# Kernel tuning notes

Measured on AMD Instinct MI355X. Metric: run time of the kernel, lower is better.

The kernel has to match this reference:

```python
import jax, jax.numpy as jnp
import numpy as np

N_NODES = 50000

def _sage(x, src, dst, Wl, bl, Wr):
    # PyG SAGEConv(aggr='mean'): out = lin_l(mean_{j in N(i)} x_j) + lin_r(x_i)
    msg = x[src]                                                    # [E, F] gather
    agg = jax.ops.segment_sum(msg, dst, num_segments=N_NODES)      # [N, F]
    cnt = jax.ops.segment_sum(jnp.ones((src.shape[0],), x.dtype), dst, num_segments=N_NODES)
    agg = agg / jnp.maximum(cnt, 1.0)[:, None]                     # mean aggregate
    return agg @ Wl + bl + x @ Wr                                   # lin_l has bias, lin_r does not


def setup_inputs() -> dict:
    key = jax.random.key(0)
    ks = jax.random.split(key, 14)
    d_in, d_h, d_out, n_edges = 128, 64, 4, 800000
    s = lambda k, shp, fan: jax.random.normal(k, shp, jnp.float32) * (1.0 / np.sqrt(fan))
    return {
        'x': jax.random.normal(ks[0], (N_NODES, d_in), jnp.float32),
        'edge_index': jax.random.randint(ks[1], (2, n_edges), 0, N_NODES, jnp.int64),
        'Wl1': s(ks[2], (d_in, d_h), d_in), 'bl1': jnp.zeros((d_h,), jnp.float32),
        'Wr1': s(ks[3], (d_in, d_h), d_in),
        'Wl2': s(ks[4], (d_h, d_h), d_h), 'bl2': jnp.zeros((d_h,), jnp.float32),
        'Wr2': s(ks[5], (d_h, d_h), d_h),
        'Wl3': s(ks[6], (d_h, d_h), d_h), 'bl3': jnp.zeros((d_h,), jnp.float32),
        'Wr3': s(ks[7], (d_h, d_h), d_h),
        'Wp': s(ks[8], (2 * d_h, d_out), 2 * d_h), 'bp': jnp.zeros((d_out,), jnp.float32),
    }


def reference(x, edge_index, Wl1, bl1, Wr1, Wl2, bl2, Wr2, Wl3, bl3, Wr3, Wp, bp):
    src, dst = edge_index[0], edge_index[1]
    # dropout is identity in eval mode
    h = jax.nn.elu(_sage(x, src, dst, Wl1, bl1, Wr1))
    h = jax.nn.elu(_sage(h, src, dst, Wl2, bl2, Wr2))
    h = jax.nn.elu(_sage(h, src, dst, Wl3, bl3, Wr3))
    edge_feat = jnp.concatenate([h[src], h[dst]], axis=1)  # [E, 2*hidden]
    return edge_feat @ Wp + bp                              # [E, output_dim]
```

## Files before the change

kernel.cpp:

```cpp
#include <hip/hip_runtime.h>
#include <hip/hip_bf16.h>

#define N_NODES 50000
#define N_EDGES 800000
#define D_IN 128
#define D_H 64
#define SCAN_BLOCKS 196
#define HIST_BLOCKS 3125
#define LIN1_BLOCKS 782
#define FRAG_BLOCKS 8
#define GL_BLOCKS 3125

#define F2L 0
#define F2R 4096
#define F3L 8192
#define F3R 12288
#define FRAG_TOTAL 16384

typedef short bf16x8 __attribute__((ext_vector_type(8)));
typedef float f32x4 __attribute__((ext_vector_type(4)));

__device__ __forceinline__ ushort f2bf(float f) {
    __hip_bfloat16 b = __float2bfloat16(f);
    return *reinterpret_cast<ushort*>(&b);
}
__device__ __forceinline__ float bf16_lo(unsigned int u) { return __uint_as_float(u << 16); }
__device__ __forceinline__ float bf16_hi(unsigned int u) { return __uint_as_float(u & 0xffff0000u); }

__device__ __forceinline__ void build_frag_one(const float* __restrict__ W, int local,
                                               ushort* __restrict__ frag, int fid) {
    int lane = local & 63;
    int ktnt = local >> 6;
    int kt = ktnt >> 2, nt = ktnt & 3;
    int quad = lane >> 4, col = lane & 15;
    ushort t0 = f2bf(W[(kt * 32 + quad * 8 + 0) * D_H + nt * 16 + col]);
    ushort t1 = f2bf(W[(kt * 32 + quad * 8 + 1) * D_H + nt * 16 + col]);
    ushort t2 = f2bf(W[(kt * 32 + quad * 8 + 2) * D_H + nt * 16 + col]);
    ushort t3 = f2bf(W[(kt * 32 + quad * 8 + 3) * D_H + nt * 16 + col]);
    ushort t4 = f2bf(W[(kt * 32 + quad * 8 + 4) * D_H + nt * 16 + col]);
    ushort t5 = f2bf(W[(kt * 32 + quad * 8 + 5) * D_H + nt * 16 + col]);
    ushort t6 = f2bf(W[(kt * 32 + quad * 8 + 6) * D_H + nt * 16 + col]);
    ushort t7 = f2bf(W[(kt * 32 + quad * 8 + 7) * D_H + nt * 16 + col]);
    uint4 v;
    v.x = (unsigned int)t0 | ((unsigned int)t1 << 16);
    v.y = (unsigned int)t2 | ((unsigned int)t3 << 16);
    v.z = (unsigned int)t4 | ((unsigned int)t5 << 16);
    v.w = (unsigned int)t6 | ((unsigned int)t7 << 16);
    *reinterpret_cast<uint4*>(frag + (size_t)fid * 8) = v;
}

__device__ __forceinline__ void lin1_body(int gwave, int lane, const float* __restrict__ hin,
                                          const ushort* fl, const ushort* fr,
                                          ushort* __restrict__ Y, ushort* __restrict__ Zb) {
    constexpr int KT = D_IN / 32;
    int m0 = gwave * 16;
    if (m0 >= N_NODES) return;
    int col = lane & 15;
    int quad = lane >> 4;

    f32x4 accl[4], accr[4];
#pragma unroll
    for (int nt = 0; nt < 4; ++nt) {
        accl[nt] = (f32x4){0.f, 0.f, 0.f, 0.f};
        accr[nt] = (f32x4){0.f, 0.f, 0.f, 0.f};
    }
    const float* arow = hin + (size_t)(m0 + col) * D_IN + quad * 8;
#pragma unroll
    for (int kt = 0; kt < KT; ++kt) {
        float4 a_lo = *reinterpret_cast<const float4*>(arow + kt * 32);
        float4 a_hi = *reinterpret_cast<const float4*>(arow + kt * 32 + 4);
        bf16x8 a;
        a[0] = (short)f2bf(a_lo.x); a[1] = (short)f2bf(a_lo.y);
        a[2] = (short)f2bf(a_lo.z); a[3] = (short)f2bf(a_lo.w);
        a[4] = (short)f2bf(a_hi.x); a[5] = (short)f2bf(a_hi.y);
        a[6] = (short)f2bf(a_hi.z); a[7] = (short)f2bf(a_hi.w);
#pragma unroll
        for (int nt = 0; nt < 4; ++nt) {
            size_t off = (size_t)((kt * 4 + nt) * 64 + lane) * 8;
            bf16x8 bl = __builtin_bit_cast(bf16x8, *reinterpret_cast<const uint4*>(fl + off));
            bf16x8 br = __builtin_bit_cast(bf16x8, *reinterpret_cast<const uint4*>(fr + off));
            accl[nt] = __builtin_amdgcn_mfma_f32_16x16x32_bf16(a, bl, accl[nt], 0, 0, 0);
            accr[nt] = __builtin_amdgcn_mfma_f32_16x16x32_bf16(a, br, accr[nt], 0, 0, 0);
        }
    }
#pragma unroll
    for (int reg = 0; reg < 4; ++reg) {
        size_t r = (size_t)(m0 + quad * 4 + reg) * D_H;
        ushort* yp = Y + r;
        ushort* zp = Zb + r;
#pragma unroll
        for (int nt = 0; nt < 4; ++nt) {
            yp[nt * 16 + col] = f2bf(accl[nt][reg]);
            zp[nt * 16 + col] = f2bf(accr[nt][reg]);
        }
    }
}

__global__ void k1_kernel(const float* __restrict__ x,
                          const float* __restrict__ Wl1, const float* __restrict__ Wr1,
                          const float* __restrict__ Wl2, const float* __restrict__ Wr2,
                          const float* __restrict__ Wl3, const float* __restrict__ Wr3,
                          const int* __restrict__ dstv, int* __restrict__ cnt,
                          ushort* __restrict__ rank, ushort* __restrict__ wfrag,
                          ushort* __restrict__ Y, ushort* __restrict__ Zb) {
    __shared__ ushort fl[8192];
    __shared__ ushort fr[8192];
    if (blockIdx.x < LIN1_BLOCKS) {
#pragma unroll
        for (int i = 0; i < 4; ++i) {
            int local = i * 256 + threadIdx.x;
            build_frag_one(Wl1, local, fl, local);
            build_frag_one(Wr1, local, fr, local);
        }
        __syncthreads();
        int gwave = (blockIdx.x * 256 + threadIdx.x) >> 6;
        lin1_body(gwave, threadIdx.x & 63, x, fl, fr, Y, Zb);
    } else if (blockIdx.x < LIN1_BLOCKS + FRAG_BLOCKS) {
        int fid = (blockIdx.x - LIN1_BLOCKS) * 256 + threadIdx.x;
        const float* W; int base;
        if (fid < 512)       { W = Wl2; base = 0; }
        else if (fid < 1024) { W = Wr2; base = 512; }
        else if (fid < 1536) { W = Wl3; base = 1024; }
        else                 { W = Wr3; base = 1536; }
        build_frag_one(W, fid - base, wfrag, fid);
    } else {
        int e = (blockIdx.x - LIN1_BLOCKS - FRAG_BLOCKS) * 256 + threadIdx.x;
        if (e < N_EDGES) {
            int r = atomicAdd(&cnt[dstv[e]], 1);
            rank[e] = (ushort)r;
        }
    }
}

__global__ void scan_partial(const int* __restrict__ cnt, int* __restrict__ blockSums) {
    __shared__ int s[256];
    int i = blockIdx.x * 256 + threadIdx.x;
    s[threadIdx.x] = (i < N_NODES) ? cnt[i] : 0;
    __syncthreads();
    for (int off = 128; off > 0; off >>= 1) {
        if (threadIdx.x < off) s[threadIdx.x] += s[threadIdx.x + off];
        __syncthreads();
    }
    if (threadIdx.x == 0) blockSums[blockIdx.x] = s[0];
}

__global__ void scan_final(const int* __restrict__ cnt, const int* __restrict__ blockSums,
                           int* __restrict__ row_ptr) {
    __shared__ int s[256];
    __shared__ int bs[256];
    int t = threadIdx.x;
    bs[t] = (t < SCAN_BLOCKS) ? blockSums[t] : 0;
    int i = blockIdx.x * 256 + t;
    s[t] = (i < N_NODES) ? cnt[i] : 0;
    __syncthreads();
    for (int off = 1; off < 256; off <<= 1) {
        int tmp1 = (t >= off) ? s[t - off] : 0;
        int tmp2 = (t >= off) ? bs[t - off] : 0;
        __syncthreads();
        s[t] += tmp1;
        bs[t] += tmp2;
        __syncthreads();
    }
    int blockExcl = (blockIdx.x > 0) ? bs[blockIdx.x - 1] : 0;
    int excl = blockExcl + ((t > 0) ? s[t - 1] : 0);
    if (i < N_NODES) row_ptr[i] = excl;
    if (i == 0) row_ptr[N_NODES] = N_EDGES;
}

__global__ void fill_kernel(const int* __restrict__ srcv, const int* __restrict__ dstv,
                            const ushort* __restrict__ rank, const int* __restrict__ row_ptr,
                            ushort* __restrict__ csr_src) {
    int e = blockIdx.x * 256 + threadIdx.x;
    if (e < N_EDGES) {
        int d = dstv[e];
        int pos = row_ptr[d] + (int)rank[e];
        csr_src[pos] = (ushort)srcv[e];
    }
}

template <bool FUSE_PROJ>
__global__ void gather_lin_kernel(const ushort* __restrict__ Y, const ushort* __restrict__ Zb,
                                  const float* __restrict__ bl,
                                  const int* __restrict__ row_ptr, const ushort* __restrict__ csr_src,
                                  const ushort* __restrict__ fragWl, const ushort* __restrict__ fragWr,
                                  ushort* __restrict__ Ynext, ushort* __restrict__ Zbnext,
                                  const float* __restrict__ Wp, const float* __restrict__ bp,
                                  float* __restrict__ ps, float* __restrict__ pd) {
    __shared__ ushort Hs[16][72];
    int w = threadIdx.x >> 6;
    int lane = threadIdx.x & 63;
    int wv = (blockIdx.x << 2) + w;
    int n0 = wv << 2;
    int g = lane >> 4;
    int l = lane & 15;

    int rp[5];
#pragma unroll
    for (int i = 0; i < 5; ++i) rp[i] = row_ptr[n0 + i];
    int deg[4];
#pragma unroll
    for (int n = 0; n < 4; ++n) deg[n] = rp[n + 1] - rp[n];
    int maxdeg = deg[0];
#pragma unroll
    for (int n = 1; n < 4; ++n) maxdeg = deg[n] > maxdeg ? deg[n] : maxdeg;

    float acc[4][4] = {{0.f}};
    const uint2* __restrict__ Y2 = reinterpret_cast<const uint2*>(Y);

    for (int base = 0; base < maxdeg; base += 64) {
        int idxv[4];
#pragma unroll
        for (int n = 0; n < 4; ++n) idxv[n] = (int)csr_src[rp[n] + base + lane];
        int wend[4];
#pragma unroll
        for (int n = 0; n < 4; ++n) { wend[n] = deg[n] - base; if (wend[n] > 64) wend[n] = 64; }
        int kmax = wend[0];
#pragma unroll
        for (int n = 1; n < 4; ++n) kmax = wend[n] > kmax ? wend[n] : kmax;
        for (int k = 0; k < kmax; k += 16) {
            uint2 rr[4][4];
#pragma unroll
            for (int n = 0; n < 4; ++n)
#pragma unroll
                for (int j = 0; j < 4; ++j) {
                    int s = __shfl(idxv[n], k + 4 * j + g);
                    rr[n][j] = Y2[s * 16 + l];
                }
#pragma unroll
            for (int n = 0; n < 4; ++n)
#pragma unroll
                for (int j = 0; j < 4; ++j) {
                    if (k + 4 * j + g < wend[n]) {
                        acc[n][0] += bf16_lo(rr[n][j].x); acc[n][1] += bf16_hi(rr[n][j].x);
                        acc[n][2] += bf16_lo(rr[n][j].y); acc[n][3] += bf16_hi(rr[n][j].y);
                    }
                }
        }
    }

#pragma unroll
    for (int n = 0; n < 4; ++n)
#pragma unroll
        for (int f = 0; f < 4; ++f) {
            acc[n][f] += __shfl_xor(acc[n][f], 16);
            acc[n][f] += __shfl_xor(acc[n][f], 32);
        }

    int node = n0 + g;
    float dgf = (g == 0) ? (float)deg[0] : (g == 1) ? (float)deg[1]
              : (g == 2) ? (float)deg[2] : (float)deg[3];
    float c0 = (g == 0) ? acc[0][0] : (g == 1) ? acc[1][0] : (g == 2) ? acc[2][0] : acc[3][0];
    float c1 = (g == 0) ? acc[0][1] : (g == 1) ? acc[1][1] : (g == 2) ? acc[2][1] : acc[3][1];
    float c2 = (g == 0) ? acc[0][2] : (g == 1) ? acc[1][2] : (g == 2) ? acc[2][2] : acc[3][2];
    float c3 = (g == 0) ? acc[0][3] : (g == 1) ? acc[1][3] : (g == 2) ? acc[2][3] : acc[3][3];
    float inv = 1.0f / fmaxf(dgf, 1.0f);
    float4 bv = reinterpret_cast<const float4*>(bl)[l];
    uint2 zr = reinterpret_cast<const uint2*>(Zb)[node * 16 + l];
    float v0 = c0 * inv + bv.x + bf16_lo(zr.x);
    float v1 = c1 * inv + bv.y + bf16_hi(zr.x);
    float v2 = c2 * inv + bv.z + bf16_lo(zr.y);
    float v3 = c3 * inv + bv.w + bf16_hi(zr.y);
    float o0 = v0 > 0.f ? v0 : expm1f(v0);
    float o1 = v1 > 0.f ? v1 : expm1f(v1);
    float o2 = v2 > 0.f ? v2 : expm1f(v2);
    float o3 = v3 > 0.f ? v3 : expm1f(v3);

    if constexpr (FUSE_PROJ) {
        float p0 = 0.f, p1 = 0.f, p2 = 0.f, p3 = 0.f;
        float q0 = 0.f, q1 = 0.f, q2 = 0.f, q3 = 0.f;
        float ov[4] = {o0, o1, o2, o3};
#pragma unroll
        for (int j = 0; j < 4; ++j) {
            int k = 4 * l + j;
            float4 wt = reinterpret_cast<const float4*>(Wp)[k];
            float4 wb = reinterpret_cast<const float4*>(Wp)[D_H + k];
            p0 += ov[j] * wt.x; p1 += ov[j] * wt.y; p2 += ov[j] * wt.z; p3 += ov[j] * wt.w;
            q0 += ov[j] * wb.x; q1 += ov[j] * wb.y; q2 += ov[j] * wb.z; q3 += ov[j] * wb.w;
        }
#pragma unroll
        for (int off = 1; off < 16; off <<= 1) {
            p0 += __shfl_xor(p0, off); p1 += __shfl_xor(p1, off);
            p2 += __shfl_xor(p2, off); p3 += __shfl_xor(p3, off);
            q0 += __shfl_xor(q0, off); q1 += __shfl_xor(q1, off);
            q2 += __shfl_xor(q2, off); q3 += __shfl_xor(q3, off);
        }
        if (l == 0) {
            float4 bpv = *reinterpret_cast<const float4*>(bp);
            float4 pv; pv.x = p0 + bpv.x; pv.y = p1 + bpv.y; pv.z = p2 + bpv.z; pv.w = p3 + bpv.w;
            float4 qv; qv.x = q0; qv.y = q1; qv.z = q2; qv.w = q3;
            reinterpret_cast<float4*>(ps)[node] = pv;
            reinterpret_cast<float4*>(pd)[node] = qv;
        }
    } else {
        ushort4 ob;
        ob.x = f2bf(o0); ob.y = f2bf(o1); ob.z = f2bf(o2); ob.w = f2bf(o3);
        int localrow = w * 4 + g;
        *reinterpret_cast<ushort4*>(&Hs[localrow][4 * l]) = ob;
        __syncthreads();

        int col = lane & 15;
        int quad = lane >> 4;
        bf16x8 blf0 = __builtin_bit_cast(bf16x8,
            *reinterpret_cast<const uint4*>(fragWl + (size_t)((0 * 4 + w) * 64 + lane) * 8));
        bf16x8 blf1 = __builtin_bit_cast(bf16x8,
            *reinterpret_cast<const uint4*>(fragWl + (size_t)((1 * 4 + w) * 64 + lane) * 8));
        bf16x8 brf0 = __builtin_bit_cast(bf16x8,
            *reinterpret_cast<const uint4*>(fragWr + (size_t)((0 * 4 + w) * 64 + lane) * 8));
        bf16x8 brf1 = __builtin_bit_cast(bf16x8,
            *reinterpret_cast<const uint4*>(fragWr + (size_t)((1 * 4 + w) * 64 + lane) * 8));
        bf16x8 a0 = __builtin_bit_cast(bf16x8,
            *reinterpret_cast<const uint4*>(&Hs[col][quad * 8]));
        bf16x8 a1 = __builtin_bit_cast(bf16x8,
            *reinterpret_cast<const uint4*>(&Hs[col][32 + quad * 8]));
        f32x4 accl = {0.f,0.f,0.f,0.f};
        f32x4 accr = {0.f,0.f,0.f,0.f};
        accl = __builtin_amdgcn_mfma_f32_16x16x32_bf16(a0, blf0, accl, 0, 0, 0);
        accl = __builtin_amdgcn_mfma_f32_16x16x32_bf16(a1, blf1, accl, 0, 0, 0);
        accr = __builtin_amdgcn_mfma_f32_16x16x32_bf16(a0, brf0, accr, 0, 0, 0);
        accr = __builtin_amdgcn_mfma_f32_16x16x32_bf16(a1, brf1, accr, 0, 0, 0);

        int n0base = blockIdx.x * 16;
#pragma unroll
        for (int reg = 0; reg < 4; ++reg) {
            size_t r = (size_t)(n0base + quad * 4 + reg) * D_H + w * 16 + col;
            Ynext[r]  = f2bf(accl[reg]);
            Zbnext[r] = f2bf(accr[reg]);
        }
    }
}

__global__ void edge_final_kernel(const int* __restrict__ srcv, const int* __restrict__ dstv,
                                  const float* __restrict__ ps, const float* __restrict__ pd,
                                  float* __restrict__ out) {
    int e = blockIdx.x * 256 + threadIdx.x;
    if (e >= N_EDGES) return;
    float4 a = reinterpret_cast<const float4*>(ps)[srcv[e]];
    float4 b = reinterpret_cast<const float4*>(pd)[dstv[e]];
    float4 o;
    o.x = a.x + b.x;
    o.y = a.y + b.y;
    o.z = a.z + b.z;
    o.w = a.w + b.w;
    reinterpret_cast<float4*>(out)[e] = o;
}

extern "C" void kernel_launch(void* const* d_in, const int* in_sizes, int n_in,
                              void* d_out, int out_size, void* d_ws, size_t ws_size,
                              hipStream_t stream) {
    const float* x   = (const float*)d_in[0];
    const int*   ei  = (const int*)d_in[1];
    const float* Wl1 = (const float*)d_in[2];
    const float* bl1 = (const float*)d_in[3];
    const float* Wr1 = (const float*)d_in[4];
    const float* Wl2 = (const float*)d_in[5];
    const float* bl2 = (const float*)d_in[6];
    const float* Wr2 = (const float*)d_in[7];
    const float* Wl3 = (const float*)d_in[8];
    const float* bl3 = (const float*)d_in[9];
    const float* Wr3 = (const float*)d_in[10];
    const float* Wp  = (const float*)d_in[11];
    const float* bp  = (const float*)d_in[12];
    float* out = (float*)d_out;

    const int* srcv = ei;
    const int* dstv = ei + N_EDGES;

    int*   cnt       = (int*)d_ws;
    int*   blockSums = cnt + 50000;
    int*   row_ptr   = blockSums + 256;
    ushort* rank     = (ushort*)(row_ptr + 50001);
    ushort* csr_src  = rank + 800000;
    ushort* wfrag = (ushort*)(((uintptr_t)(csr_src + 800000 + 4096) + 127) & ~(uintptr_t)127);
    ushort* Y1  = (ushort*)(((uintptr_t)(wfrag + FRAG_TOTAL) + 127) & ~(uintptr_t)127);
    ushort* Zb1 = Y1 + (size_t)N_NODES * D_H;
    ushort* Y2  = Zb1 + (size_t)N_NODES * D_H;
    ushort* Zb2 = Y2 + (size_t)N_NODES * D_H;
    float* ps = (float*)(((uintptr_t)(Zb2 + (size_t)N_NODES * D_H) + 15) & ~(uintptr_t)15);
    float* pd = ps + (size_t)N_NODES * 4;

    hipMemsetAsync(cnt, 0, N_NODES * sizeof(int), stream);
    k1_kernel<<<LIN1_BLOCKS + FRAG_BLOCKS + HIST_BLOCKS, 256, 0, stream>>>(
        x, Wl1, Wr1, Wl2, Wr2, Wl3, Wr3, dstv, cnt, rank, wfrag, Y1, Zb1);

    scan_partial<<<SCAN_BLOCKS, 256, 0, stream>>>(cnt, blockSums);
    scan_final<<<SCAN_BLOCKS, 256, 0, stream>>>(cnt, blockSums, row_ptr);

    fill_kernel<<<HIST_BLOCKS, 256, 0, stream>>>(srcv, dstv, rank, row_ptr, csr_src);

    gather_lin_kernel<false><<<GL_BLOCKS, 256, 0, stream>>>(Y1, Zb1, bl1, row_ptr, csr_src,
                                                            wfrag + F2L, wfrag + F2R, Y2, Zb2,
                                                            nullptr, nullptr, nullptr, nullptr);

    gather_lin_kernel<false><<<GL_BLOCKS, 256, 0, stream>>>(Y2, Zb2, bl2, row_ptr, csr_src,
                                                            wfrag + F3L, wfrag + F3R, Y1, Zb1,
                                                            nullptr, nullptr, nullptr, nullptr);

    gather_lin_kernel<true><<<GL_BLOCKS, 256, 0, stream>>>(Y1, Zb1, bl3, row_ptr, csr_src,
                                                           nullptr, nullptr, nullptr, nullptr,
                                                           Wp, bp, ps, pd);

    edge_final_kernel<<<(N_EDGES + 255) / 256, 256, 0, stream>>>(srcv, dstv, ps, pd, out);
}
```

Measured before the change: 228.5 us.

## Sort nodes by degree bucket for balanced gather waves; split lin1 fragment staging

Builds a degree histogram and a counting-sort permutation of nodes into 64 degree buckets, and makes the gather/linear kernels process nodes in that permuted order. Each wave then handles four nodes of similar degree, which cuts divergence where lanes idle until the max degree in the group finishes. Outputs are scattered back through the permutation, which costs extra indirection and makes row writes non-contiguous. The layer-1 kernel also stages weight fragments in two halves to halve its shared memory, adding one more barrier.

```diff
diff --git a/kernel.cpp b/kernel.cpp
--- a/kernel.cpp
+++ b/kernel.cpp
@@ -10,6 +10,7 @@
 #define LIN1_BLOCKS 782
 #define FRAG_BLOCKS 8
 #define GL_BLOCKS 3125
+#define NBUCKET 64
 
 #define F2L 0
 #define F2R 4096
@@ -27,20 +28,17 @@
 __device__ __forceinline__ float bf16_lo(unsigned int u) { return __uint_as_float(u << 16); }
 __device__ __forceinline__ float bf16_hi(unsigned int u) { return __uint_as_float(u & 0xffff0000u); }
 
-__device__ __forceinline__ void build_frag_one(const float* __restrict__ W, int local,
-                                               ushort* __restrict__ frag, int fid) {
-    int lane = local & 63;
-    int ktnt = local >> 6;
-    int kt = ktnt >> 2, nt = ktnt & 3;
+__device__ __forceinline__ void build_frag_kt(const float* __restrict__ W, int ktA, int nt,
+                                              int lane, ushort* __restrict__ frag, int fid) {
     int quad = lane >> 4, col = lane & 15;
-    ushort t0 = f2bf(W[(kt * 32 + quad * 8 + 0) * D_H + nt * 16 + col]);
-    ushort t1 = f2bf(W[(kt * 32 + quad * 8 + 1) * D_H + nt * 16 + col]);
-    ushort t2 = f2bf(W[(kt * 32 + quad * 8 + 2) * D_H + nt * 16 + col]);
-    ushort t3 = f2bf(W[(kt * 32 + quad * 8 + 3) * D_H + nt * 16 + col]);
-    ushort t4 = f2bf(W[(kt * 32 + quad * 8 + 4) * D_H + nt * 16 + col]);
-    ushort t5 = f2bf(W[(kt * 32 + quad * 8 + 5) * D_H + nt * 16 + col]);
-    ushort t6 = f2bf(W[(kt * 32 + quad * 8 + 6) * D_H + nt * 16 + col]);
-    ushort t7 = f2bf(W[(kt * 32 + quad * 8 + 7) * D_H + nt * 16 + col]);
+    ushort t0 = f2bf(W[(ktA * 32 + quad * 8 + 0) * D_H + nt * 16 + col]);
+    ushort t1 = f2bf(W[(ktA * 32 + quad * 8 + 1) * D_H + nt * 16 + col]);
+    ushort t2 = f2bf(W[(ktA * 32 + quad * 8 + 2) * D_H + nt * 16 + col]);
+    ushort t3 = f2bf(W[(ktA * 32 + quad * 8 + 3) * D_H + nt * 16 + col]);
+    ushort t4 = f2bf(W[(ktA * 32 + quad * 8 + 4) * D_H + nt * 16 + col]);
+    ushort t5 = f2bf(W[(ktA * 32 + quad * 8 + 5) * D_H + nt * 16 + col]);
+    ushort t6 = f2bf(W[(ktA * 32 + quad * 8 + 6) * D_H + nt * 16 + col]);
+    ushort t7 = f2bf(W[(ktA * 32 + quad * 8 + 7) * D_H + nt * 16 + col]);
     uint4 v;
     v.x = (unsigned int)t0 | ((unsigned int)t1 << 16);
     v.y = (unsigned int)t2 | ((unsigned int)t3 << 16);
@@ -49,51 +47,11 @@
     *reinterpret_cast<uint4*>(frag + (size_t)fid * 8) = v;
 }
 
-__device__ __forceinline__ void lin1_body(int gwave, int lane, const float* __restrict__ hin,
-                                          const ushort* fl, const ushort* fr,
-                                          ushort* __restrict__ Y, ushort* __restrict__ Zb) {
-    constexpr int KT = D_IN / 32;
-    int m0 = gwave * 16;
-    if (m0 >= N_NODES) return;
-    int col = lane & 15;
-    int quad = lane >> 4;
-
-    f32x4 accl[4], accr[4];
-#pragma unroll
-    for (int nt = 0; nt < 4; ++nt) {
-        accl[nt] = (f32x4){0.f, 0.f, 0.f, 0.f};
-        accr[nt] = (f32x4){0.f, 0.f, 0.f, 0.f};
-    }
-    const float* arow = hin + (size_t)(m0 + col) * D_IN + quad * 8;
-#pragma unroll
-    for (int kt = 0; kt < KT; ++kt) {
-        float4 a_lo = *reinterpret_cast<const float4*>(arow + kt * 32);
-        float4 a_hi = *reinterpret_cast<const float4*>(arow + kt * 32 + 4);
-        bf16x8 a;
-        a[0] = (short)f2bf(a_lo.x); a[1] = (short)f2bf(a_lo.y);
-        a[2] = (short)f2bf(a_lo.z); a[3] = (short)f2bf(a_lo.w);
-        a[4] = (short)f2bf(a_hi.x); a[5] = (short)f2bf(a_hi.y);
-        a[6] = (short)f2bf(a_hi.z); a[7] = (short)f2bf(a_hi.w);
-#pragma unroll
-        for (int nt = 0; nt < 4; ++nt) {
-            size_t off = (size_t)((kt * 4 + nt) * 64 + lane) * 8;
-            bf16x8 bl = __builtin_bit_cast(bf16x8, *reinterpret_cast<const uint4*>(fl + off));
-            bf16x8 br = __builtin_bit_cast(bf16x8, *reinterpret_cast<const uint4*>(fr + off));
-            accl[nt] = __builtin_amdgcn_mfma_f32_16x16x32_bf16(a, bl, accl[nt], 0, 0, 0);
-            accr[nt] = __builtin_amdgcn_mfma_f32_16x16x32_bf16(a, br, accr[nt], 0, 0, 0);
-        }
-    }
-#pragma unroll
-    for (int reg = 0; reg < 4; ++reg) {
-        size_t r = (size_t)(m0 + quad * 4 + reg) * D_H;
-        ushort* yp = Y + r;
-        ushort* zp = Zb + r;
-#pragma unroll
-        for (int nt = 0; nt < 4; ++nt) {
-            yp[nt * 16 + col] = f2bf(accl[nt][reg]);
-            zp[nt * 16 + col] = f2bf(accr[nt][reg]);
-        }
-    }
+__device__ __forceinline__ void build_frag_one(const float* __restrict__ W, int local,
+                                               ushort* __restrict__ frag, int fid) {
+    int lane = local & 63;
+    int ktnt = local >> 6;
+    build_frag_kt(W, ktnt >> 2, ktnt & 3, lane, frag, fid);
 }
 
 __global__ void k1_kernel(const float* __restrict__ x,
@@ -103,18 +61,69 @@
                           const int* __restrict__ dstv, int* __restrict__ cnt,
                           ushort* __restrict__ rank, ushort* __restrict__ wfrag,
                           ushort* __restrict__ Y, ushort* __restrict__ Zb) {
-    __shared__ ushort fl[8192];
-    __shared__ ushort fr[8192];
+    __shared__ ushort fl[4096];
+    __shared__ ushort fr[4096];
     if (blockIdx.x < LIN1_BLOCKS) {
-#pragma unroll
-        for (int i = 0; i < 4; ++i) {
-            int local = i * 256 + threadIdx.x;
-            build_frag_one(Wl1, local, fl, local);
-            build_frag_one(Wr1, local, fr, local);
-        }
-        __syncthreads();
-        int gwave = (blockIdx.x * 256 + threadIdx.x) >> 6;
-        lin1_body(gwave, threadIdx.x & 63, x, fl, fr, Y, Zb);
+        int tid = threadIdx.x;
+        int lane = tid & 63;
+        int gwave = (blockIdx.x * 256 + tid) >> 6;
+        int m0 = gwave * 16;
+        int col = lane & 15;
+        int quad = lane >> 4;
+        f32x4 accl[4], accr[4];
+#pragma unroll
+        for (int nt = 0; nt < 4; ++nt) {
+            accl[nt] = (f32x4){0.f, 0.f, 0.f, 0.f};
+            accr[nt] = (f32x4){0.f, 0.f, 0.f, 0.f};
+        }
+        const float* arow = x + (size_t)(m0 + col) * D_IN + quad * 8;
+#pragma unroll
+        for (int s = 0; s < 2; ++s) {
+#pragma unroll
+            for (int i = 0; i < 2; ++i) {
+                int local = i * 256 + tid;
+                int ktnt = local >> 6;
+                int kt_l = ktnt >> 2, nt = ktnt & 3;
+                build_frag_kt(Wl1, 2 * s + kt_l, nt, local & 63, fl, local);
+                build_frag_kt(Wr1, 2 * s + kt_l, nt, local & 63, fr, local);
+            }
+            __syncthreads();
+            if (m0 < N_NODES) {
+#pragma unroll
+                for (int kt_l = 0; kt_l < 2; ++kt_l) {
+                    int ktA = 2 * s + kt_l;
+                    float4 a_lo = *reinterpret_cast<const float4*>(arow + ktA * 32);
+                    float4 a_hi = *reinterpret_cast<const float4*>(arow + ktA * 32 + 4);
+                    bf16x8 a;
+                    a[0] = (short)f2bf(a_lo.x); a[1] = (short)f2bf(a_lo.y);
+                    a[2] = (short)f2bf(a_lo.z); a[3] = (short)f2bf(a_lo.w);
+                    a[4] = (short)f2bf(a_hi.x); a[5] = (short)f2bf(a_hi.y);
+                    a[6] = (short)f2bf(a_hi.z); a[7] = (short)f2bf(a_hi.w);
+#pragma unroll
+                    for (int nt = 0; nt < 4; ++nt) {
+                        size_t off = (size_t)((kt_l * 4 + nt) * 64 + lane) * 8;
+                        bf16x8 bl = __builtin_bit_cast(bf16x8, *reinterpret_cast<const uint4*>(fl + off));
+                        bf16x8 br = __builtin_bit_cast(bf16x8, *reinterpret_cast<const uint4*>(fr + off));
+                        accl[nt] = __builtin_amdgcn_mfma_f32_16x16x32_bf16(a, bl, accl[nt], 0, 0, 0);
+                        accr[nt] = __builtin_amdgcn_mfma_f32_16x16x32_bf16(a, br, accr[nt], 0, 0, 0);
+                    }
+                }
+            }
+            if (s == 0) __syncthreads();
+        }
+        if (m0 < N_NODES) {
+#pragma unroll
+            for (int reg = 0; reg < 4; ++reg) {
+                size_t r = (size_t)(m0 + quad * 4 + reg) * D_H;
+                ushort* yp = Y + r;
+                ushort* zp = Zb + r;
+#pragma unroll
+                for (int nt = 0; nt < 4; ++nt) {
+                    yp[nt * 16 + col] = f2bf(accl[nt][reg]);
+                    zp[nt * 16 + col] = f2bf(accr[nt][reg]);
+                }
+            }
+        }
     } else if (blockIdx.x < LIN1_BLOCKS + FRAG_BLOCKS) {
         int fid = (blockIdx.x - LIN1_BLOCKS) * 256 + threadIdx.x;
         const float* W; int base;
@@ -132,11 +141,21 @@
     }
 }
 
-__global__ void scan_partial(const int* __restrict__ cnt, int* __restrict__ blockSums) {
+__global__ void scan_partial(const int* __restrict__ cnt, int* __restrict__ blockSums,
+                             int* __restrict__ dhist) {
     __shared__ int s[256];
+    __shared__ int h[NBUCKET];
     int i = blockIdx.x * 256 + threadIdx.x;
-    s[threadIdx.x] = (i < N_NODES) ? cnt[i] : 0;
+    int v = (i < N_NODES) ? cnt[i] : 0;
+    s[threadIdx.x] = v;
+    if (threadIdx.x < NBUCKET) h[threadIdx.x] = 0;
     __syncthreads();
+    if (i < N_NODES) {
+        int b = v < (NBUCKET - 1) ? v : (NBUCKET - 1);
+        atomicAdd(&h[b], 1);
+    }
+    __syncthreads();
+    if (threadIdx.x < NBUCKET) atomicAdd(&dhist[threadIdx.x], h[threadIdx.x]);
     for (int off = 128; off > 0; off >>= 1) {
         if (threadIdx.x < off) s[threadIdx.x] += s[threadIdx.x + off];
         __syncthreads();
@@ -145,26 +164,43 @@
 }
 
 __global__ void scan_final(const int* __restrict__ cnt, const int* __restrict__ blockSums,
-                           int* __restrict__ row_ptr) {
+                           const int* __restrict__ dhist, int* __restrict__ dcur,
+                           int* __restrict__ row_ptr, int* __restrict__ perm) {
     __shared__ int s[256];
     __shared__ int bs[256];
+    __shared__ int db[NBUCKET];
     int t = threadIdx.x;
-    bs[t] = (t < SCAN_BLOCKS) ? blockSums[t] : 0;
-    int i = blockIdx.x * 256 + t;
-    s[t] = (i < N_NODES) ? cnt[i] : 0;
-    __syncthreads();
-    for (int off = 1; off < 256; off <<= 1) {
-        int tmp1 = (t >= off) ? s[t - off] : 0;
-        int tmp2 = (t >= off) ? bs[t - off] : 0;
+    if (blockIdx.x < SCAN_BLOCKS) {
+        bs[t] = (t < SCAN_BLOCKS) ? blockSums[t] : 0;
+        int i = blockIdx.x * 256 + t;
+        s[t] = (i < N_NODES) ? cnt[i] : 0;
         __syncthreads();
-        s[t] += tmp1;
-        bs[t] += tmp2;
+        for (int off = 1; off < 256; off <<= 1) {
+            int tmp1 = (t >= off) ? s[t - off] : 0;
+            int tmp2 = (t >= off) ? bs[t - off] : 0;
+            __syncthreads();
+            s[t] += tmp1;
+            bs[t] += tmp2;
+            __syncthreads();
+        }
+        int blockExcl = (blockIdx.x > 0) ? bs[blockIdx.x - 1] : 0;
+        int excl = blockExcl + ((t > 0) ? s[t - 1] : 0);
+        if (i < N_NODES) row_ptr[i] = excl;
+        if (i == 0) row_ptr[N_NODES] = N_EDGES;
+    } else {
+        if (t == 0) {
+            int run = 0;
+            for (int j = 0; j < NBUCKET; ++j) { db[j] = run; run += dhist[j]; }
+        }
         __syncthreads();
-    }
-    int blockExcl = (blockIdx.x > 0) ? bs[blockIdx.x - 1] : 0;
-    int excl = blockExcl + ((t > 0) ? s[t - 1] : 0);
-    if (i < N_NODES) row_ptr[i] = excl;
-    if (i == 0) row_ptr[N_NODES] = N_EDGES;
+        int i = (blockIdx.x - SCAN_BLOCKS) * 256 + t;
+        if (i < N_NODES) {
+            int v = cnt[i];
+            int b = v < (NBUCKET - 1) ? v : (NBUCKET - 1);
+            int pos = db[b] + atomicAdd(&dcur[b], 1);
+            perm[pos] = i;
+        }
+    }
 }
 
 __global__ void fill_kernel(const int* __restrict__ srcv, const int* __restrict__ dstv,
@@ -182,11 +218,13 @@
 __global__ void gather_lin_kernel(const ushort* __restrict__ Y, const ushort* __restrict__ Zb,
                                   const float* __restrict__ bl,
                                   const int* __restrict__ row_ptr, const ushort* __restrict__ csr_src,
+                                  const int* __restrict__ perm,
                                   const ushort* __restrict__ fragWl, const ushort* __restrict__ fragWr,
                                   ushort* __restrict__ Ynext, ushort* __restrict__ Zbnext,
                                   const float* __restrict__ Wp, const float* __restrict__ bp,
                                   float* __restrict__ ps, float* __restrict__ pd) {
     __shared__ ushort Hs[16][72];
+    __shared__ int nids[16];
     int w = threadIdx.x >> 6;
     int lane = threadIdx.x & 63;
     int wv = (blockIdx.x << 2) + w;
@@ -194,12 +232,15 @@
     int g = lane >> 4;
     int l = lane & 15;
 
-    int rp[5];
-#pragma unroll
-    for (int i = 0; i < 5; ++i) rp[i] = row_ptr[n0 + i];
-    int deg[4];
-#pragma unroll
-    for (int n = 0; n < 4; ++n) deg[n] = rp[n + 1] - rp[n];
+    int nid[4];
+#pragma unroll
+    for (int n = 0; n < 4; ++n) nid[n] = perm[n0 + n];
+    int rplo[4], deg[4];
+#pragma unroll
+    for (int n = 0; n < 4; ++n) {
+        rplo[n] = row_ptr[nid[n]];
+        deg[n] = row_ptr[nid[n] + 1] - rplo[n];
+    }
     int maxdeg = deg[0];
 #pragma unroll
     for (int n = 1; n < 4; ++n) maxdeg = deg[n] > maxdeg ? deg[n] : maxdeg;
@@ -210,7 +251,7 @@
     for (int base = 0; base < maxdeg; base += 64) {
         int idxv[4];
 #pragma unroll
-        for (int n = 0; n < 4; ++n) idxv[n] = (int)csr_src[rp[n] + base + lane];
+        for (int n = 0; n < 4; ++n) idxv[n] = (int)csr_src[rplo[n] + base + lane];
         int wend[4];
 #pragma unroll
         for (int n = 0; n < 4; ++n) { wend[n] = deg[n] - base; if (wend[n] > 64) wend[n] = 64; }
@@ -246,7 +287,7 @@
             acc[n][f] += __shfl_xor(acc[n][f], 32);
         }
 
-    int node = n0 + g;
+    int node = (g == 0) ? nid[0] : (g == 1) ? nid[1] : (g == 2) ? nid[2] : nid[3];
     float dgf = (g == 0) ? (float)deg[0] : (g == 1) ? (float)deg[1]
               : (g == 2) ? (float)deg[2] : (float)deg[3];
     float c0 = (g == 0) ? acc[0][0] : (g == 1) ? acc[1][0] : (g == 2) ? acc[2][0] : acc[3][0];
@@ -296,6 +337,7 @@
         ob.x = f2bf(o0); ob.y = f2bf(o1); ob.z = f2bf(o2); ob.w = f2bf(o3);
         int localrow = w * 4 + g;
         *reinterpret_cast<ushort4*>(&Hs[localrow][4 * l]) = ob;
+        if (l == 0) nids[localrow] = node;
         __syncthreads();
 
         int col = lane & 15;
@@ -319,10 +361,10 @@
         accr = __builtin_amdgcn_mfma_f32_16x16x32_bf16(a0, brf0, accr, 0, 0, 0);
         accr = __builtin_amdgcn_mfma_f32_16x16x32_bf16(a1, brf1, accr, 0, 0, 0);
 
-        int n0base = blockIdx.x * 16;
 #pragma unroll
         for (int reg = 0; reg < 4; ++reg) {
-            size_t r = (size_t)(n0base + quad * 4 + reg) * D_H + w * 16 + col;
+            int orow = nids[quad * 4 + reg];
+            size_t r = (size_t)orow * D_H + w * 16 + col;
             Ynext[r]  = f2bf(accl[reg]);
             Zbnext[r] = f2bf(accr[reg]);
         }
@@ -366,9 +408,12 @@
     const int* dstv = ei + N_EDGES;
 
     int*   cnt       = (int*)d_ws;
-    int*   blockSums = cnt + 50000;
+    int*   dhist     = cnt + 50000;
+    int*   dcur      = dhist + 64;
+    int*   blockSums = dcur + 64;
     int*   row_ptr   = blockSums + 256;
-    ushort* rank     = (ushort*)(row_ptr + 50001);
+    int*   perm      = row_ptr + 50001;
+    ushort* rank     = (ushort*)(perm + 50000);
     ushort* csr_src  = rank + 800000;
     ushort* wfrag = (ushort*)(((uintptr_t)(csr_src + 800000 + 4096) + 127) & ~(uintptr_t)127);
     ushort* Y1  = (ushort*)(((uintptr_t)(wfrag + FRAG_TOTAL) + 127) & ~(uintptr_t)127);
@@ -378,24 +423,24 @@
     float* ps = (float*)(((uintptr_t)(Zb2 + (size_t)N_NODES * D_H) + 15) & ~(uintptr_t)15);
     float* pd = ps + (size_t)N_NODES * 4;
 
-    hipMemsetAsync(cnt, 0, N_NODES * sizeof(int), stream);
+    hipMemsetAsync(cnt, 0, (50000 + 128) * sizeof(int), stream);
     k1_kernel<<<LIN1_BLOCKS + FRAG_BLOCKS + HIST_BLOCKS, 256, 0, stream>>>(
         x, Wl1, Wr1, Wl2, Wr2, Wl3, Wr3, dstv, cnt, rank, wfrag, Y1, Zb1);
 
-    scan_partial<<<SCAN_BLOCKS, 256, 0, stream>>>(cnt, blockSums);
-    scan_final<<<SCAN_BLOCKS, 256, 0, stream>>>(cnt, blockSums, row_ptr);
+    scan_partial<<<SCAN_BLOCKS, 256, 0, stream>>>(cnt, blockSums, dhist);
+    scan_final<<<2 * SCAN_BLOCKS, 256, 0, stream>>>(cnt, blockSums, dhist, dcur, row_ptr, perm);
 
     fill_kernel<<<HIST_BLOCKS, 256, 0, stream>>>(srcv, dstv, rank, row_ptr, csr_src);
 
-    gather_lin_kernel<false><<<GL_BLOCKS, 256, 0, stream>>>(Y1, Zb1, bl1, row_ptr, csr_src,
+    gather_lin_kernel<false><<<GL_BLOCKS, 256, 0, stream>>>(Y1, Zb1, bl1, row_ptr, csr_src, perm,
                                                             wfrag + F2L, wfrag + F2R, Y2, Zb2,
                                                             nullptr, nullptr, nullptr, nullptr);
 
-    gather_lin_kernel<false><<<GL_BLOCKS, 256, 0, stream>>>(Y2, Zb2, bl2, row_ptr, csr_src,
+    gather_lin_kernel<false><<<GL_BLOCKS, 256, 0, stream>>>(Y2, Zb2, bl2, row_ptr, csr_src, perm,
                                                             wfrag + F3L, wfrag + F3R, Y1, Zb1,
                                                             nullptr, nullptr, nullptr, nullptr);
 
-    gather_lin_kernel<true><<<GL_BLOCKS, 256, 0, stream>>>(Y1, Zb1, bl3, row_ptr, csr_src,
+    gather_lin_kernel<true><<<GL_BLOCKS, 256, 0, stream>>>(Y1, Zb1, bl3, row_ptr, csr_src, perm,
                                                            nullptr, nullptr, nullptr, nullptr,
                                                            Wp, bp, ps, pd);
 
```

Result: slower. 339.2 us (+48.4%).

## Stage layer-1 weight fragments in two K halves and predicate gather accumulation

Applied to the files above, without the earlier changes.

The first-layer GEMM blocks now build the bf16 weight fragments in two K-halves, using half the shared memory, and interleave fragment construction with the MFMA work. The goal is higher occupancy and earlier start of compute in the lin1 path, at the cost of an extra barrier. In the aggregation kernel, the branchy conditional adds become mask-multiplied FMAs to avoid divergence. The bias and Zb loads are also hoisted ahead of the cross-lane reductions so their latency overlaps the shuffles.

```diff
diff --git a/kernel.cpp b/kernel.cpp
--- a/kernel.cpp
+++ b/kernel.cpp
@@ -27,20 +27,17 @@
 __device__ __forceinline__ float bf16_lo(unsigned int u) { return __uint_as_float(u << 16); }
 __device__ __forceinline__ float bf16_hi(unsigned int u) { return __uint_as_float(u & 0xffff0000u); }
 
-__device__ __forceinline__ void build_frag_one(const float* __restrict__ W, int local,
-                                               ushort* __restrict__ frag, int fid) {
-    int lane = local & 63;
-    int ktnt = local >> 6;
-    int kt = ktnt >> 2, nt = ktnt & 3;
+__device__ __forceinline__ void build_frag_kt(const float* __restrict__ W, int ktA, int nt,
+                                              int lane, ushort* __restrict__ frag, int fid) {
     int quad = lane >> 4, col = lane & 15;
-    ushort t0 = f2bf(W[(kt * 32 + quad * 8 + 0) * D_H + nt * 16 + col]);
-    ushort t1 = f2bf(W[(kt * 32 + quad * 8 + 1) * D_H + nt * 16 + col]);
-    ushort t2 = f2bf(W[(kt * 32 + quad * 8 + 2) * D_H + nt * 16 + col]);
-    ushort t3 = f2bf(W[(kt * 32 + quad * 8 + 3) * D_H + nt * 16 + col]);
-    ushort t4 = f2bf(W[(kt * 32 + quad * 8 + 4) * D_H + nt * 16 + col]);
-    ushort t5 = f2bf(W[(kt * 32 + quad * 8 + 5) * D_H + nt * 16 + col]);
-    ushort t6 = f2bf(W[(kt * 32 + quad * 8 + 6) * D_H + nt * 16 + col]);
-    ushort t7 = f2bf(W[(kt * 32 + quad * 8 + 7) * D_H + nt * 16 + col]);
+    ushort t0 = f2bf(W[(ktA * 32 + quad * 8 + 0) * D_H + nt * 16 + col]);
+    ushort t1 = f2bf(W[(ktA * 32 + quad * 8 + 1) * D_H + nt * 16 + col]);
+    ushort t2 = f2bf(W[(ktA * 32 + quad * 8 + 2) * D_H + nt * 16 + col]);
+    ushort t3 = f2bf(W[(ktA * 32 + quad * 8 + 3) * D_H + nt * 16 + col]);
+    ushort t4 = f2bf(W[(ktA * 32 + quad * 8 + 4) * D_H + nt * 16 + col]);
+    ushort t5 = f2bf(W[(ktA * 32 + quad * 8 + 5) * D_H + nt * 16 + col]);
+    ushort t6 = f2bf(W[(ktA * 32 + quad * 8 + 6) * D_H + nt * 16 + col]);
+    ushort t7 = f2bf(W[(ktA * 32 + quad * 8 + 7) * D_H + nt * 16 + col]);
     uint4 v;
     v.x = (unsigned int)t0 | ((unsigned int)t1 << 16);
     v.y = (unsigned int)t2 | ((unsigned int)t3 << 16);
@@ -49,51 +46,11 @@
     *reinterpret_cast<uint4*>(frag + (size_t)fid * 8) = v;
 }
 
-__device__ __forceinline__ void lin1_body(int gwave, int lane, const float* __restrict__ hin,
-                                          const ushort* fl, const ushort* fr,
-                                          ushort* __restrict__ Y, ushort* __restrict__ Zb) {
-    constexpr int KT = D_IN / 32;
-    int m0 = gwave * 16;
-    if (m0 >= N_NODES) return;
-    int col = lane & 15;
-    int quad = lane >> 4;
-
-    f32x4 accl[4], accr[4];
-#pragma unroll
-    for (int nt = 0; nt < 4; ++nt) {
-        accl[nt] = (f32x4){0.f, 0.f, 0.f, 0.f};
-        accr[nt] = (f32x4){0.f, 0.f, 0.f, 0.f};
-    }
-    const float* arow = hin + (size_t)(m0 + col) * D_IN + quad * 8;
-#pragma unroll
-    for (int kt = 0; kt < KT; ++kt) {
-        float4 a_lo = *reinterpret_cast<const float4*>(arow + kt * 32);
-        float4 a_hi = *reinterpret_cast<const float4*>(arow + kt * 32 + 4);
-        bf16x8 a;
-        a[0] = (short)f2bf(a_lo.x); a[1] = (short)f2bf(a_lo.y);
-        a[2] = (short)f2bf(a_lo.z); a[3] = (short)f2bf(a_lo.w);
-        a[4] = (short)f2bf(a_hi.x); a[5] = (short)f2bf(a_hi.y);
-        a[6] = (short)f2bf(a_hi.z); a[7] = (short)f2bf(a_hi.w);
-#pragma unroll
-        for (int nt = 0; nt < 4; ++nt) {
-            size_t off = (size_t)((kt * 4 + nt) * 64 + lane) * 8;
-            bf16x8 bl = __builtin_bit_cast(bf16x8, *reinterpret_cast<const uint4*>(fl + off));
-            bf16x8 br = __builtin_bit_cast(bf16x8, *reinterpret_cast<const uint4*>(fr + off));
-            accl[nt] = __builtin_amdgcn_mfma_f32_16x16x32_bf16(a, bl, accl[nt], 0, 0, 0);
-            accr[nt] = __builtin_amdgcn_mfma_f32_16x16x32_bf16(a, br, accr[nt], 0, 0, 0);
-        }
-    }
-#pragma unroll
-    for (int reg = 0; reg < 4; ++reg) {
-        size_t r = (size_t)(m0 + quad * 4 + reg) * D_H;
-        ushort* yp = Y + r;
-        ushort* zp = Zb + r;
-#pragma unroll
-        for (int nt = 0; nt < 4; ++nt) {
-            yp[nt * 16 + col] = f2bf(accl[nt][reg]);
-            zp[nt * 16 + col] = f2bf(accr[nt][reg]);
-        }
-    }
+__device__ __forceinline__ void build_frag_one(const float* __restrict__ W, int local,
+                                               ushort* __restrict__ frag, int fid) {
+    int lane = local & 63;
+    int ktnt = local >> 6;
+    build_frag_kt(W, ktnt >> 2, ktnt & 3, lane, frag, fid);
 }
 
 __global__ void k1_kernel(const float* __restrict__ x,
@@ -103,18 +60,69 @@
                           const int* __restrict__ dstv, int* __restrict__ cnt,
                           ushort* __restrict__ rank, ushort* __restrict__ wfrag,
                           ushort* __restrict__ Y, ushort* __restrict__ Zb) {
-    __shared__ ushort fl[8192];
-    __shared__ ushort fr[8192];
+    __shared__ ushort fl[4096];
+    __shared__ ushort fr[4096];
     if (blockIdx.x < LIN1_BLOCKS) {
-#pragma unroll
-        for (int i = 0; i < 4; ++i) {
-            int local = i * 256 + threadIdx.x;
-            build_frag_one(Wl1, local, fl, local);
-            build_frag_one(Wr1, local, fr, local);
-        }
-        __syncthreads();
-        int gwave = (blockIdx.x * 256 + threadIdx.x) >> 6;
-        lin1_body(gwave, threadIdx.x & 63, x, fl, fr, Y, Zb);
+        int tid = threadIdx.x;
+        int lane = tid & 63;
+        int gwave = (blockIdx.x * 256 + tid) >> 6;
+        int m0 = gwave * 16;
+        int col = lane & 15;
+        int quad = lane >> 4;
+        f32x4 accl[4], accr[4];
+#pragma unroll
+        for (int nt = 0; nt < 4; ++nt) {
+            accl[nt] = (f32x4){0.f, 0.f, 0.f, 0.f};
+            accr[nt] = (f32x4){0.f, 0.f, 0.f, 0.f};
+        }
+        const float* arow = x + (size_t)(m0 + col) * D_IN + quad * 8;
+#pragma unroll
+        for (int s = 0; s < 2; ++s) {
+#pragma unroll
+            for (int i = 0; i < 2; ++i) {
+                int local = i * 256 + tid;
+                int ktnt = local >> 6;
+                int kt_l = ktnt >> 2, nt = ktnt & 3;
+                build_frag_kt(Wl1, 2 * s + kt_l, nt, local & 63, fl, local);
+                build_frag_kt(Wr1, 2 * s + kt_l, nt, local & 63, fr, local);
+            }
+            __syncthreads();
+            if (m0 < N_NODES) {
+#pragma unroll
+                for (int kt_l = 0; kt_l < 2; ++kt_l) {
+                    int ktA = 2 * s + kt_l;
+                    float4 a_lo = *reinterpret_cast<const float4*>(arow + ktA * 32);
+                    float4 a_hi = *reinterpret_cast<const float4*>(arow + ktA * 32 + 4);
+                    bf16x8 a;
+                    a[0] = (short)f2bf(a_lo.x); a[1] = (short)f2bf(a_lo.y);
+                    a[2] = (short)f2bf(a_lo.z); a[3] = (short)f2bf(a_lo.w);
+                    a[4] = (short)f2bf(a_hi.x); a[5] = (short)f2bf(a_hi.y);
+                    a[6] = (short)f2bf(a_hi.z); a[7] = (short)f2bf(a_hi.w);
+#pragma unroll
+                    for (int nt = 0; nt < 4; ++nt) {
+                        size_t off = (size_t)((kt_l * 4 + nt) * 64 + lane) * 8;
+                        bf16x8 bl = __builtin_bit_cast(bf16x8, *reinterpret_cast<const uint4*>(fl + off));
+                        bf16x8 br = __builtin_bit_cast(bf16x8, *reinterpret_cast<const uint4*>(fr + off));
+                        accl[nt] = __builtin_amdgcn_mfma_f32_16x16x32_bf16(a, bl, accl[nt], 0, 0, 0);
+                        accr[nt] = __builtin_amdgcn_mfma_f32_16x16x32_bf16(a, br, accr[nt], 0, 0, 0);
+                    }
+                }
+            }
+            if (s == 0) __syncthreads();
+        }
+        if (m0 < N_NODES) {
+#pragma unroll
+            for (int reg = 0; reg < 4; ++reg) {
+                size_t r = (size_t)(m0 + quad * 4 + reg) * D_H;
+                ushort* yp = Y + r;
+                ushort* zp = Zb + r;
+#pragma unroll
+                for (int nt = 0; nt < 4; ++nt) {
+                    yp[nt * 16 + col] = f2bf(accl[nt][reg]);
+                    zp[nt * 16 + col] = f2bf(accr[nt][reg]);
+                }
+            }
+        }
     } else if (blockIdx.x < LIN1_BLOCKS + FRAG_BLOCKS) {
         int fid = (blockIdx.x - LIN1_BLOCKS) * 256 + threadIdx.x;
         const float* W; int base;
@@ -230,13 +238,18 @@
             for (int n = 0; n < 4; ++n)
 #pragma unroll
                 for (int j = 0; j < 4; ++j) {
-                    if (k + 4 * j + g < wend[n]) {
-                        acc[n][0] += bf16_lo(rr[n][j].x); acc[n][1] += bf16_hi(rr[n][j].x);
-                        acc[n][2] += bf16_lo(rr[n][j].y); acc[n][3] += bf16_hi(rr[n][j].y);
-                    }
+                    float m = (k + 4 * j + g < wend[n]) ? 1.0f : 0.0f;
+                    acc[n][0] = fmaf(m, bf16_lo(rr[n][j].x), acc[n][0]);
+                    acc[n][1] = fmaf(m, bf16_hi(rr[n][j].x), acc[n][1]);
+                    acc[n][2] = fmaf(m, bf16_lo(rr[n][j].y), acc[n][2]);
+                    acc[n][3] = fmaf(m, bf16_hi(rr[n][j].y), acc[n][3]);
                 }
         }
     }
+
+    int node = n0 + g;
+    float4 bv = reinterpret_cast<const float4*>(bl)[l];
+    uint2 zr = reinterpret_cast<const uint2*>(Zb)[node * 16 + l];
 
 #pragma unroll
     for (int n = 0; n < 4; ++n)
@@ -246,7 +259,6 @@
             acc[n][f] += __shfl_xor(acc[n][f], 32);
         }
 
-    int node = n0 + g;
     float dgf = (g == 0) ? (float)deg[0] : (g == 1) ? (float)deg[1]
               : (g == 2) ? (float)deg[2] : (float)deg[3];
     float c0 = (g == 0) ? acc[0][0] : (g == 1) ? acc[1][0] : (g == 2) ? acc[2][0] : acc[3][0];
@@ -254,8 +266,6 @@
     float c2 = (g == 0) ? acc[0][2] : (g == 1) ? acc[1][2] : (g == 2) ? acc[2][2] : acc[3][2];
     float c3 = (g == 0) ? acc[0][3] : (g == 1) ? acc[1][3] : (g == 2) ? acc[2][3] : acc[3][3];
     float inv = 1.0f / fmaxf(dgf, 1.0f);
-    float4 bv = reinterpret_cast<const float4*>(bl)[l];
-    uint2 zr = reinterpret_cast<const uint2*>(Zb)[node * 16 + l];
     float v0 = c0 * inv + bv.x + bf16_lo(zr.x);
     float v1 = c1 * inv + bv.y + bf16_hi(zr.x);
     float v2 = c2 * inv + bv.z + bf16_lo(zr.y);
```

After: 229.1 us. About the same (+0.2%).
